# Optimization experiments

Hardware: AMD Instinct MI355X
Metric: run time of the kernel (lower is better)

## Reference

```python
import jax, jax.numpy as jnp
import numpy as np

B, L, D_MODEL, H, D_K, D_V, C = 4, 2048, 512, 8, 64, 64, 5
LN_EPS = 1e-5


def setup_inputs() -> dict:
    key = jax.random.key(0)
    ks = jax.random.split(key, 9)
    u_k = min(int(C * np.log(L)), L)  # 38
    s = 1.0 / np.sqrt(D_MODEL)
    return {
        "input_Q": jax.random.normal(ks[0], (B, L, D_MODEL), jnp.float32),
        "input_K": jax.random.normal(ks[1], (B, L, D_MODEL), jnp.float32),
        "input_V": jax.random.normal(ks[2], (B, L, D_MODEL), jnp.float32),
        "W_Q": jax.random.normal(ks[3], (D_MODEL, H * D_K), jnp.float32) * s,
        "W_K": jax.random.normal(ks[4], (D_MODEL, H * D_K), jnp.float32) * s,
        "W_V": jax.random.normal(ks[5], (D_MODEL, H * D_V), jnp.float32) * s,
        "W_fc": jax.random.normal(ks[6], (H * D_V, D_MODEL), jnp.float32) * (1.0 / np.sqrt(H * D_V)),
        "ln_gamma": jnp.ones((D_MODEL,), jnp.float32),
        "ln_beta": jnp.zeros((D_MODEL,), jnp.float32),
        "index_sample": jax.random.randint(ks[7], (L, u_k), 0, L, jnp.int32),
    }


def reference(input_Q, input_K, input_V, W_Q, W_K, W_V, W_fc, ln_gamma, ln_beta, index_sample):
    Bb, L_Q, _ = input_Q.shape
    L_K = input_K.shape[1]
    u_q = min(int(C * np.log(L_Q)), L_Q)  # n_top queries kept

    # projections -> (B, H, L, d)
    Q = (input_Q @ W_Q).reshape(Bb, L_Q, H, D_K).transpose(0, 2, 1, 3)
    K = (input_K @ W_K).reshape(Bb, L_K, H, D_K).transpose(0, 2, 1, 3)
    V = (input_V @ W_V).reshape(Bb, L_K, H, D_V).transpose(0, 2, 1, 3)

    # sampled QK scores: gather u_k random keys per query position
    K_sample = K[:, :, index_sample, :]                      # (B,H,L_Q,u_k,d_k)
    QK_sample = jnp.einsum('bhqe,bhqke->bhqk', Q, K_sample)  # (B,H,L_Q,u_k)

    # sparsity measure M = max - mean, top-u_q queries
    M = QK_sample.max(axis=-1) - QK_sample.mean(axis=-1)     # (B,H,L_Q)
    _, idx = jax.lax.top_k(M, u_q)                           # (B,H,u_q)

    # attention only for selected queries
    Q_sel = jnp.take_along_axis(Q, idx[..., None], axis=2)   # (B,H,u_q,d_k)
    scores = jnp.einsum('bhue,bhke->bhuk', Q_sel, K) / np.sqrt(D_K)
    attn = jax.nn.softmax(scores, axis=-1)
    values = jnp.einsum('bhuk,bhkd->bhud', attn, V)          # (B,H,u_q,d_v)

    # initial context = mean of V (attn_mask is None), scatter selected rows
    context = jnp.broadcast_to(V.mean(axis=2, keepdims=True), (Bb, H, L_Q, D_V))
    bb = jnp.arange(Bb)[:, None, None]
    hh = jnp.arange(H)[None, :, None]
    context = context.at[bb, hh, idx].set(values)

    context = context.transpose(0, 2, 1, 3).reshape(Bb, L_Q, H * D_V)
    out = context @ W_fc                                     # dropout p=0.0

    y = out + input_Q
    mu = y.mean(axis=-1, keepdims=True)
    var = jnp.mean(jnp.square(y - mu), axis=-1, keepdims=True)
    y = (y - mu) / jnp.sqrt(var + LN_EPS) * ln_gamma + ln_beta
    return y, idx
```

## Files before the change

kernel.cpp:

```cpp
#include <hip/hip_runtime.h>
#include <hip/hip_bf16.h>

#define NB 4
#define NL 2048
#define NH 8
#define NDM 512
#define ND 64
#define KSPLIT 4
#define QB 8

typedef __attribute__((ext_vector_type(8))) short short8b;
typedef __attribute__((ext_vector_type(4))) float f32x4;

__global__ void samp_flag_init(int* __restrict__ flag) {
  if (threadIdx.x == 0 && blockIdx.x == 0) *flag = 0;
}
__global__ void samp_probe(const int* __restrict__ sampAsInt, int* __restrict__ flag, int nwords) {
  const int g = blockIdx.x * 256 + threadIdx.x;
  if (g < nwords) {
    unsigned v = (unsigned)sampAsInt[g];
    if (v >= 2048u) atomicOr(flag, 1);
  }
}
__global__ void samp_convert(const void* __restrict__ samp, const int* __restrict__ flag,
                             int* __restrict__ sampI, int n) {
  const int g = blockIdx.x * 256 + threadIdx.x;
  if (g >= n) return;
  int v;
  if (*flag == 0) v = ((const int*)samp)[g];
  else            v = (int)(((const float*)samp)[g]);
  if (v < 0) v = 0;
  if (v > NL - 1) v = NL - 1;
  sampI[g] = v;
}

__global__ void wconv(const float* __restrict__ W, unsigned short* __restrict__ WT) {
  const int g = blockIdx.x * 256 + threadIdx.x;
  const int k = g >> 9, c = g & 511;
  __hip_bfloat16 hb = __float2bfloat16(W[(size_t)k * 512 + c]);
  WT[(size_t)c * 512 + k] = *reinterpret_cast<unsigned short*>(&hb);
}

__global__ void vmean_colmean(const float* __restrict__ inV, float* __restrict__ parts) {
  const int b = blockIdx.x, seg = blockIdx.y, t = threadIdx.x;
  const float* p = inV + ((size_t)b * NL + seg * 32) * NDM;
  float s0 = 0.f, s1 = 0.f;
  for (int r = 0; r < 32; ++r) {
    s0 += p[(size_t)r * NDM + t];
    s1 += p[(size_t)r * NDM + 256 + t];
  }
  parts[((size_t)b * 64 + seg) * NDM + t] = s0;
  parts[((size_t)b * 64 + seg) * NDM + 256 + t] = s1;
}
__global__ void vmean_gemm(const float* __restrict__ parts, const float* __restrict__ Wv,
                           float* __restrict__ Vm) {
  __shared__ float cm[512];
  const int b = blockIdx.x, t = threadIdx.x;
  float a0 = 0.f, a1 = 0.f;
  for (int g = 0; g < 64; ++g) {
    a0 += parts[((size_t)b * 64 + g) * NDM + t];
    a1 += parts[((size_t)b * 64 + g) * NDM + 256 + t];
  }
  cm[t] = a0 * (1.f / 2048.f);
  cm[t + 256] = a1 * (1.f / 2048.f);
  __syncthreads();
  const int c0 = blockIdx.y * 256 + t;
  float acc = 0.f;
  for (int k = 0; k < 512; ++k) acc += cm[k] * Wv[(size_t)k * NDM + c0];
  Vm[b * 512 + c0] = acc;
}

__global__ __launch_bounds__(256, 4) void proj3(
    const float* __restrict__ AQ, const float* __restrict__ AK,
    const float* __restrict__ wQm, const float* __restrict__ wKm,
    int gh0, float* __restrict__ Qc, float* __restrict__ Kc) {
  __shared__ float As_[32 * 132];
  __shared__ float Ws_[32 * 68];
  const int tid = threadIdx.x;
  const int bm = blockIdx.x;
  const int hl = blockIdx.y;
  const int mat = blockIdx.z;
  const int bh = gh0 + hl;
  const int b = bh >> 3, h = bh & 7;
  const float* A = (mat == 0) ? AQ : AK;
  const float* W = (mat == 0) ? wQm : wKm;
  float* D = (mat == 0) ? Qc : Kc;
  const float* Ab = A + (size_t)b * NL * NDM;
  const int colbase = h * 64;
  const int tm = tid >> 4, tn = tid & 15;
  float acc[8][4] = {};
  for (int k0 = 0; k0 < 512; k0 += 32) {
#pragma unroll
    for (int i = 0; i < 4; ++i) {
      int s = tid + i * 256;
      int r = s >> 3, c4 = (s & 7) * 4;
      float4 v = *reinterpret_cast<const float4*>(Ab + (size_t)(bm * 128 + r) * 512 + k0 + c4);
      float vv[4] = {v.x, v.y, v.z, v.w};
#pragma unroll
      for (int j = 0; j < 4; ++j) {
        int c = c4 + j;
        int rs = r ^ (((c >> 2) & 3) << 3);
        As_[c * 132 + rs] = vv[j];
      }
    }
#pragma unroll
    for (int i = 0; i < 2; ++i) {
      int s = tid + i * 256;
      int r = s >> 4, c4 = (s & 15) * 4;
      *reinterpret_cast<float4*>(&Ws_[r * 68 + c4]) =
          *reinterpret_cast<const float4*>(W + (size_t)(k0 + r) * 512 + colbase + c4);
    }
    __syncthreads();
#pragma unroll
    for (int kk = 0; kk < 32; ++kk) {
      const int sw = ((kk >> 2) & 3) << 3;
      const int mbase = (tm * 4) ^ sw;
      float4 a0 = *reinterpret_cast<const float4*>(&As_[kk * 132 + mbase]);
      float4 a1 = *reinterpret_cast<const float4*>(&As_[kk * 132 + 64 + mbase]);
      float4 w  = *reinterpret_cast<const float4*>(&Ws_[kk * 68 + tn * 4]);
      float a[8] = {a0.x, a0.y, a0.z, a0.w, a1.x, a1.y, a1.z, a1.w};
      float wv[4] = {w.x, w.y, w.z, w.w};
#pragma unroll
      for (int ii = 0; ii < 8; ++ii)
#pragma unroll
        for (int jj = 0; jj < 4; ++jj) acc[ii][jj] += a[ii] * wv[jj];
    }
    __syncthreads();
  }
#pragma unroll
  for (int ii = 0; ii < 8; ++ii) {
    int row = bm * 128 + ((ii < 4) ? (tm * 4 + ii) : (64 + tm * 4 + (ii - 4)));
    float4 v = make_float4(acc[ii][0], acc[ii][1], acc[ii][2], acc[ii][3]);
    *reinterpret_cast<float4*>(D + ((size_t)hl * NL + row) * ND + tn * 4) = v;
  }
}

__global__ __launch_bounds__(256) void projV_mfma(
    const float* __restrict__ AV, const unsigned short* __restrict__ WT,
    int gh0, float* __restrict__ Vc) {
  const int wv = threadIdx.x >> 6, l = threadIdx.x & 63;
  const int bm = blockIdx.x;
  const int hl = blockIdx.y;
  const int bh = gh0 + hl;
  const int b = bh >> 3, h = bh & 7;
  const float* Ab = AV + (size_t)b * NL * NDM;
  const int row = bm * 64 + wv * 16 + (l & 15);
  const int kg = (l >> 4) * 8;
  f32x4 acc0 = {}, acc1 = {}, acc2 = {}, acc3 = {};
  for (int k0 = 0; k0 < 512; k0 += 32) {
    const float* ap = Ab + (size_t)row * 512 + k0 + kg;
    short8b af;
#pragma unroll
    for (int j = 0; j < 8; ++j) {
      __hip_bfloat16 hb = __float2bfloat16(ap[j]);
      af[j] = *reinterpret_cast<short*>(&hb);
    }
    const unsigned short* wp = WT + (size_t)(h * 64 + (l & 15)) * 512 + k0 + kg;
    short8b b0 = *reinterpret_cast<const short8b*>(wp);
    short8b b1 = *reinterpret_cast<const short8b*>(wp + 16 * 512);
    short8b b2 = *reinterpret_cast<const short8b*>(wp + 32 * 512);
    short8b b3 = *reinterpret_cast<const short8b*>(wp + 48 * 512);
    acc0 = __builtin_amdgcn_mfma_f32_16x16x32_bf16(af, b0, acc0, 0, 0, 0);
    acc1 = __builtin_amdgcn_mfma_f32_16x16x32_bf16(af, b1, acc1, 0, 0, 0);
    acc2 = __builtin_amdgcn_mfma_f32_16x16x32_bf16(af, b2, acc2, 0, 0, 0);
    acc3 = __builtin_amdgcn_mfma_f32_16x16x32_bf16(af, b3, acc3, 0, 0, 0);
  }
  const int rbase = bm * 64 + wv * 16 + (l >> 4) * 4;
  const int col = l & 15;
#pragma unroll
  for (int j = 0; j < 4; ++j) {
    size_t o = ((size_t)hl * NL + rbase + j) * ND + col;
    Vc[o] = acc0[j];
    Vc[o + 16] = acc1[j];
    Vc[o + 32] = acc2[j];
    Vc[o + 48] = acc3[j];
  }
}

template <int UK>
__global__ __launch_bounds__(256) void sample_scores_t(
    const float* __restrict__ Q, const float* __restrict__ K,
    const int* __restrict__ sampI, float* __restrict__ M) {
  __shared__ float KsAll[4][UK * 66];
  __shared__ float QsAll[4][68];
  const int wv = threadIdx.x >> 6, l = threadIdx.x & 63;
  const int gq = blockIdx.x * 4 + wv;
  const int hl = gq >> 11;
  const int q = gq & 2047;
  float* Ks = KsAll[wv];
  float* Qs = QsAll[wv];
  const float* Kb = K + (size_t)hl * NL * ND;
  Qs[l] = Q[(size_t)gq * ND + l];
  const int base = __builtin_amdgcn_readfirstlane(q) * UK;
#pragma unroll
  for (int r = 0; r < UK; ++r) {
    int kk = sampI[base + r] & (NL - 1);
    Ks[r * 66 + l] = Kb[(size_t)kk * ND + l];
  }
  __syncthreads();
  const int myk = (l < UK) ? l : (UK - 1);
  float acc = 0.f;
#pragma unroll
  for (int j = 0; j < 32; ++j) {
    float2 kv = *reinterpret_cast<const float2*>(&Ks[myk * 66 + 2 * j]);
    float2 qv = *reinterpret_cast<const float2*>(&Qs[2 * j]);
    acc += kv.x * qv.x + kv.y * qv.y;
  }
  float mval = (l < UK) ? acc : -1e30f;
  float sval = (l < UK) ? acc : 0.f;
#pragma unroll
  for (int o = 32; o; o >>= 1) {
    mval = fmaxf(mval, __shfl_xor(mval, o, 64));
    sval += __shfl_xor(sval, o, 64);
  }
  if (l == 0) M[gq] = mval - sval * (1.f / (float)UK);
}

__global__ void sample_scores_gen(const float* __restrict__ Q, const float* __restrict__ K,
                                  const int* __restrict__ sampI, float* __restrict__ M, int uk) {
  const int wave = threadIdx.x >> 6, lane = threadIdx.x & 63;
  const int gq = blockIdx.x * 4 + wave;
  const int hl = gq >> 11;
  const int q = gq & 2047;
  const float qv = Q[(size_t)gq * ND + lane];
  const float* Kbase = K + (size_t)hl * NL * ND;
  float mx = -1e30f, sm = 0.f;
  for (int k = 0; k < uk; ++k) {
    int kidx = sampI[q * uk + k] & (NL - 1);
    float p = qv * Kbase[(size_t)kidx * ND + lane];
#pragma unroll
    for (int o = 32; o; o >>= 1) p += __shfl_xor(p, o, 64);
    mx = fmaxf(mx, p);
    sm += p;
  }
  if (lane == 0) M[gq] = mx - sm / (float)uk;
}

__global__ void topk_kernel(const float* __restrict__ M, int* __restrict__ idxo,
                            float* __restrict__ outIdx, int uq) {
  __shared__ float mv[2048];
  __shared__ float bwv[4];
  __shared__ int bwi[4];
  const int bh = blockIdx.x, t = threadIdx.x;
  for (int i = 0; i < 8; ++i) mv[t + i * 256] = M[(size_t)bh * 2048 + t + i * 256];
  __syncthreads();
  for (int it = 0; it < uq; ++it) {
    float best = -1e38f; int bidx = 1 << 30;
#pragma unroll
    for (int i = 0; i < 8; ++i) {
      int id = t + i * 256;
      float v = mv[id];
      if (v > best || (v == best && id < bidx)) { best = v; bidx = id; }
    }
#pragma unroll
    for (int o = 32; o; o >>= 1) {
      float ov = __shfl_xor(best, o, 64);
      int oi = __shfl_xor(bidx, o, 64);
      if (ov > best || (ov == best && oi < bidx)) { best = ov; bidx = oi; }
    }
    if ((t & 63) == 0) { bwv[t >> 6] = best; bwi[t >> 6] = bidx; }
    __syncthreads();
    if (t == 0) {
      float bb = bwv[0]; int bi2 = bwi[0];
#pragma unroll
      for (int w = 1; w < 4; ++w) {
        if (bwv[w] > bb || (bwv[w] == bb && bwi[w] < bi2)) { bb = bwv[w]; bi2 = bwi[w]; }
      }
      int sel = bi2 & (NL - 1);
      idxo[bh * uq + it] = sel;
      outIdx[bh * uq + it] = (float)sel;
      mv[sel] = -1e38f;
    }
    __syncthreads();
  }
}

__global__ __launch_bounds__(256) void attn_part(
    const float* __restrict__ Qw, const float* __restrict__ Kw, const float* __restrict__ Vw,
    const int* __restrict__ idxo, float* __restrict__ pacc, float* __restrict__ pml, int uq) {
  __shared__ float Qs[QB][68];
  __shared__ float Ks[64][68];
  __shared__ float Vs[64][68];
  __shared__ float sc[QB][66];
  __shared__ float accs[QB][68];
  const int hl = blockIdx.x, qg = blockIdx.y, ks = blockIdx.z;
  const int t = threadIdx.x;
#pragma unroll
  for (int i = 0; i < 2; ++i) {
    int s = t + i * 256;
    int q = s >> 6, d = s & 63;
    int u = qg * QB + q;
    float v = 0.f;
    if (u < uq) {
      int qi = idxo[hl * uq + u] & (NL - 1);
      v = Qw[((size_t)hl * NL + qi) * ND + d];
    }
    Qs[q][d] = v;
    accs[q][d] = 0.f;
  }
  float m_run = -1e30f, l_run = 0.f;
  const int q2 = t >> 5, ln = t & 31;
  __syncthreads();
  const int kbeg = ks * (NL / KSPLIT);
  for (int k0 = kbeg; k0 < kbeg + NL / KSPLIT; k0 += 64) {
#pragma unroll
    for (int i = 0; i < 4; ++i) {
      int s = t + i * 256;
      int r = s >> 4, c4 = (s & 15) * 4;
      *reinterpret_cast<float4*>(&Ks[r][c4]) =
          *reinterpret_cast<const float4*>(Kw + ((size_t)hl * NL + k0 + r) * ND + c4);
      *reinterpret_cast<float4*>(&Vs[r][c4]) =
          *reinterpret_cast<const float4*>(Vw + ((size_t)hl * NL + k0 + r) * ND + c4);
    }
    __syncthreads();
    {
      const int q = t & 7, kk = t >> 3;
      float d0 = 0.f, d1 = 0.f;
#pragma unroll
      for (int dd = 0; dd < 64; dd += 4) {
        float4 qv = *reinterpret_cast<const float4*>(&Qs[q][dd]);
        float4 ka = *reinterpret_cast<const float4*>(&Ks[kk][dd]);
        float4 kb = *reinterpret_cast<const float4*>(&Ks[kk + 32][dd]);
        d0 += qv.x * ka.x + qv.y * ka.y + qv.z * ka.z + qv.w * ka.w;
        d1 += qv.x * kb.x + qv.y * kb.y + qv.z * kb.z + qv.w * kb.w;
      }
      sc[q][kk] = d0 * 0.125f;
      sc[q][kk + 32] = d1 * 0.125f;
    }
    __syncthreads();
    {
      float s0 = sc[q2][ln], s1 = sc[q2][ln + 32];
      float tmax = fmaxf(s0, s1);
#pragma unroll
      for (int o = 16; o; o >>= 1) tmax = fmaxf(tmax, __shfl_xor(tmax, o, 64));
      float mnew = fmaxf(m_run, tmax);
      float scl = __expf(m_run - mnew);
      float p0 = __expf(s0 - mnew), p1 = __expf(s1 - mnew);
      float tsum = p0 + p1;
#pragma unroll
      for (int o = 16; o; o >>= 1) tsum += __shfl_xor(tsum, o, 64);
      l_run = l_run * scl + tsum;
      m_run = mnew;
      sc[q2][ln] = p0; sc[q2][ln + 32] = p1;
      float a0 = accs[q2][2 * ln] * scl, a1 = accs[q2][2 * ln + 1] * scl;
#pragma unroll 8
      for (int k = 0; k < 64; ++k) {
        float p = sc[q2][k];
        a0 += p * Vs[k][2 * ln];
        a1 += p * Vs[k][2 * ln + 1];
      }
      accs[q2][2 * ln] = a0; accs[q2][2 * ln + 1] = a1;
    }
    __syncthreads();
  }
  const int u = qg * QB + q2;
  if (u < uq) {
    size_t g = ((size_t)hl * uq + u) * KSPLIT + ks;
    pacc[g * ND + 2 * ln] = accs[q2][2 * ln];
    pacc[g * ND + 2 * ln + 1] = accs[q2][2 * ln + 1];
    if (ln == 0) { pml[g * 2] = m_run; pml[g * 2 + 1] = l_run; }
  }
}

__global__ void attn_merge(const float* __restrict__ pacc, const float* __restrict__ pml,
                           float* __restrict__ vals, int uq) {
  const int g = blockIdx.x;
  const int d = threadIdx.x;
  float mstar = -1e30f;
#pragma unroll
  for (int s = 0; s < KSPLIT; ++s) mstar = fmaxf(mstar, pml[((size_t)g * KSPLIT + s) * 2]);
  float num = 0.f, den = 0.f;
#pragma unroll
  for (int s = 0; s < KSPLIT; ++s) {
    float e = __expf(pml[((size_t)g * KSPLIT + s) * 2] - mstar);
    den += e * pml[((size_t)g * KSPLIT + s) * 2 + 1];
    num += e * pacc[((size_t)g * KSPLIT + s) * ND + d];
  }
  vals[(size_t)g * ND + d] = num / den;
}

__global__ void selmap_init(short* __restrict__ selmap) {
  const int g = blockIdx.x * 256 + threadIdx.x;
  selmap[g] = -1;
  selmap[g + 32768] = -1;
}
__global__ void selmap_fill(const int* __restrict__ idxo, short* __restrict__ selmap, int uq) {
  const int g = blockIdx.x * 256 + threadIdx.x;
  if (g >= NB * NH * uq) return;
  const int bh = g / uq, u = g - bh * uq;
  const int b = bh >> 3, h = bh & 7;
  const int l = idxo[g] & (NL - 1);
  selmap[((size_t)b * NL + l) * NH + h] = (short)u;
}

__global__ void base_gemm(const float* __restrict__ Vm, const float* __restrict__ Wfc,
                          float* __restrict__ base) {
  __shared__ float vm[512];
  const int b = blockIdx.x, t = threadIdx.x;
  vm[t] = Vm[b * 512 + t];
  vm[t + 256] = Vm[b * 512 + t + 256];
  __syncthreads();
  const int c0 = blockIdx.y * 256 + t;
  float acc = 0.f;
  for (int k = 0; k < 512; ++k) acc += vm[k] * Wfc[(size_t)k * 512 + c0];
  base[b * 512 + c0] = acc;
}

__global__ void corr_gemm(const float* __restrict__ vals, const float* __restrict__ Vm,
                          const float* __restrict__ Wfc, float* __restrict__ corr, int uq) {
  __shared__ float diff[64];
  const int g = blockIdx.x, t = threadIdx.x;
  const int bh = g / uq;
  const int h = bh & 7;
  if (t < 64) diff[t] = vals[(size_t)g * 64 + t] - Vm[bh * 64 + t];
  __syncthreads();
  float a0 = 0.f, a1 = 0.f;
#pragma unroll
  for (int d = 0; d < 64; ++d) {
    a0 += diff[d] * Wfc[(size_t)(h * 64 + d) * 512 + t];
    a1 += diff[d] * Wfc[(size_t)(h * 64 + d) * 512 + t + 256];
  }
  corr[(size_t)g * 512 + t] = a0;
  corr[(size_t)g * 512 + t + 256] = a1;
}

__global__ void ln_fused(const float* __restrict__ base, const float* __restrict__ resid,
                         const float* __restrict__ corr, const short* __restrict__ selmap,
                         const float* __restrict__ gamma, const float* __restrict__ beta,
                         float* __restrict__ out, int uq) {
  __shared__ float red[256];
  const int row = blockIdx.x, t = threadIdx.x;
  const int b = row >> 11;
  float y0 = base[b * 512 + t] + resid[(size_t)row * 512 + t];
  float y1 = base[b * 512 + 256 + t] + resid[(size_t)row * 512 + 256 + t];
#pragma unroll
  for (int h = 0; h < NH; ++h) {
    int s = selmap[(size_t)row * NH + h];
    if (s >= 0 && s < uq) {
      const float* cp = corr + (size_t)((b * NH + h) * uq + s) * 512;
      y0 += cp[t];
      y1 += cp[t + 256];
    }
  }
  red[t] = y0 + y1;
  __syncthreads();
  for (int s = 128; s; s >>= 1) { if (t < s) red[t] += red[t + s]; __syncthreads(); }
  const float mu = red[0] * (1.f / 512.f);
  __syncthreads();
  const float d0 = y0 - mu, d1 = y1 - mu;
  red[t] = d0 * d0 + d1 * d1;
  __syncthreads();
  for (int s = 128; s; s >>= 1) { if (t < s) red[t] += red[t + s]; __syncthreads(); }
  const float rs = rsqrtf(red[0] * (1.f / 512.f) + 1e-5f);
  __syncthreads();
  out[(size_t)row * 512 + t] = d0 * rs * gamma[t] + beta[t];
  out[(size_t)row * 512 + 256 + t] = d1 * rs * gamma[256 + t] + beta[256 + t];
}

extern "C" void kernel_launch(void* const* d_in, const int* in_sizes, int n_in,
                              void* d_out, int out_size, void* d_ws, size_t ws_size,
                              hipStream_t stream) {
  const float* inQ = (const float*)d_in[0];
  const float* inK = (const float*)d_in[1];
  const float* inV = (const float*)d_in[2];
  const float* wQ = (const float*)d_in[3];
  const float* wK = (const float*)d_in[4];
  const float* wV = (const float*)d_in[5];
  const float* wFC = (const float*)d_in[6];
  const float* gamma = (const float*)d_in[7];
  const float* beta = (const float*)d_in[8];
  const void* samp = d_in[9];

  const int nsamp = in_sizes[9];
  const int uk = nsamp / NL;
  const int uq = uk;
  const int nqg = (uq + QB - 1) / QB;

  if (out_size < NB * NL * NDM + NB * NH * uq) return;

  const size_t perH = 3 * 131072 + 2048 + (size_t)uq * KSPLIT * 64 + (size_t)uq * KSPLIT * 2;
  const size_t fixed = (size_t)32 * uq * 64 + 2048 + 2048 + (size_t)32 * uq * 512
                     + (size_t)32 * uq + 32768 + (size_t)nsamp + 131072 + 131072 + 256;
  int hcg = 0;
  for (int c = 32; c >= 1; c >>= 1) {
    if ((perH * (size_t)c + fixed + 256) * 4ull <= ws_size) { hcg = c; break; }
  }
  if (hcg == 0) return;

  float* ws = (float*)d_ws;
  float* Qc = ws;
  float* Kc = Qc + (size_t)hcg * 131072;
  float* Vc = Kc + (size_t)hcg * 131072;
  float* Mb = Vc + (size_t)hcg * 131072;
  float* pacc = Mb + (size_t)hcg * 2048;
  float* pml = pacc + (size_t)hcg * uq * KSPLIT * 64;
  float* vals = pml + (size_t)hcg * uq * KSPLIT * 2;
  float* Vm = vals + (size_t)32 * uq * 64;
  float* base = Vm + 2048;
  float* corr = base + 2048;
  int* idxo = (int*)(corr + (size_t)32 * uq * 512);
  short* selmap = (short*)(idxo + (size_t)32 * uq);
  int* sampI = (int*)(selmap + 65536);
  int* flag = sampI + nsamp;
  unsigned short* WTv = (unsigned short*)(flag + 64);
  float* vparts = (float*)(WTv + 262144);

  float* out = (float*)d_out;
  float* outIdx = out + (size_t)NB * NL * NDM;

  const int nwords = nsamp / 2;
  samp_flag_init<<<1, 64, 0, stream>>>(flag);
  samp_probe<<<(nwords + 255) / 256, 256, 0, stream>>>((const int*)samp, flag, nwords);
  samp_convert<<<(nsamp + 255) / 256, 256, 0, stream>>>(samp, flag, sampI, nsamp);
  wconv<<<1024, 256, 0, stream>>>(wV, WTv);
  vmean_colmean<<<dim3(NB, 64), 256, 0, stream>>>(inV, vparts);
  vmean_gemm<<<dim3(NB, 2), 256, 0, stream>>>(vparts, wV, Vm);

  for (int gh0 = 0; gh0 < NB * NH; gh0 += hcg) {
    proj3<<<dim3(16, hcg, 2), 256, 0, stream>>>(inQ, inK, wQ, wK, gh0, Qc, Kc);
    projV_mfma<<<dim3(32, hcg), 256, 0, stream>>>(inV, WTv, gh0, Vc);
    if (uk == 38)
      sample_scores_t<38><<<hcg * NL / 4, 256, 0, stream>>>(Qc, Kc, sampI, Mb);
    else
      sample_scores_gen<<<hcg * NL / 4, 256, 0, stream>>>(Qc, Kc, sampI, Mb, uk);
    topk_kernel<<<hcg, 256, 0, stream>>>(Mb, idxo + (size_t)gh0 * uq,
                                         outIdx + (size_t)gh0 * uq, uq);
    attn_part<<<dim3(hcg, nqg, KSPLIT), 256, 0, stream>>>(Qc, Kc, Vc,
                                                          idxo + (size_t)gh0 * uq,
                                                          pacc, pml, uq);
    attn_merge<<<hcg * uq, 64, 0, stream>>>(pacc, pml, vals + (size_t)gh0 * uq * ND, uq);
  }

  selmap_init<<<NB * NL * NH / 2 / 256, 256, 0, stream>>>(selmap);
  selmap_fill<<<(NB * NH * uq + 255) / 256, 256, 0, stream>>>(idxo, selmap, uq);
  base_gemm<<<dim3(NB, 2), 256, 0, stream>>>(Vm, wFC, base);
  corr_gemm<<<NB * NH * uq, 256, 0, stream>>>(vals, Vm, wFC, corr, uq);
  ln_fused<<<NB * NL, 256, 0, stream>>>(base, inQ, corr, selmap, gamma, beta, out, uq);
}
```

Measured before the change: 380.0 us.

## Drop sample-index conversion kernels, double attention key split, remove LDS swizzle

Removes the three preprocessing launches that checked whether index_sample was stored as int or float, clamped it and copied it. The sampling kernels now read the raw int32 input directly, masked to the valid range. Separately, KSPLIT goes from 4 to 8 to give the split-key attention more blocks, and the XOR swizzle in the proj3 shared-memory A tile is removed. Removing the swizzle may bring back LDS bank conflicts, and the larger split adds partial results for the merge kernel to combine.

```diff
diff --git a/kernel.cpp b/kernel.cpp
--- a/kernel.cpp
+++ b/kernel.cpp
@@ -6,33 +6,11 @@
 #define NH 8
 #define NDM 512
 #define ND 64
-#define KSPLIT 4
+#define KSPLIT 8
 #define QB 8
 
 typedef __attribute__((ext_vector_type(8))) short short8b;
 typedef __attribute__((ext_vector_type(4))) float f32x4;
-
-__global__ void samp_flag_init(int* __restrict__ flag) {
-  if (threadIdx.x == 0 && blockIdx.x == 0) *flag = 0;
-}
-__global__ void samp_probe(const int* __restrict__ sampAsInt, int* __restrict__ flag, int nwords) {
-  const int g = blockIdx.x * 256 + threadIdx.x;
-  if (g < nwords) {
-    unsigned v = (unsigned)sampAsInt[g];
-    if (v >= 2048u) atomicOr(flag, 1);
-  }
-}
-__global__ void samp_convert(const void* __restrict__ samp, const int* __restrict__ flag,
-                             int* __restrict__ sampI, int n) {
-  const int g = blockIdx.x * 256 + threadIdx.x;
-  if (g >= n) return;
-  int v;
-  if (*flag == 0) v = ((const int*)samp)[g];
-  else            v = (int)(((const float*)samp)[g]);
-  if (v < 0) v = 0;
-  if (v > NL - 1) v = NL - 1;
-  sampI[g] = v;
-}
 
 __global__ void wconv(const float* __restrict__ W, unsigned short* __restrict__ WT) {
   const int g = blockIdx.x * 256 + threadIdx.x;
@@ -95,13 +73,10 @@
       int s = tid + i * 256;
       int r = s >> 3, c4 = (s & 7) * 4;
       float4 v = *reinterpret_cast<const float4*>(Ab + (size_t)(bm * 128 + r) * 512 + k0 + c4);
-      float vv[4] = {v.x, v.y, v.z, v.w};
-#pragma unroll
-      for (int j = 0; j < 4; ++j) {
-        int c = c4 + j;
-        int rs = r ^ (((c >> 2) & 3) << 3);
-        As_[c * 132 + rs] = vv[j];
-      }
+      As_[(c4 + 0) * 132 + r] = v.x;
+      As_[(c4 + 1) * 132 + r] = v.y;
+      As_[(c4 + 2) * 132 + r] = v.z;
+      As_[(c4 + 3) * 132 + r] = v.w;
     }
 #pragma unroll
     for (int i = 0; i < 2; ++i) {
@@ -113,10 +88,8 @@
     __syncthreads();
 #pragma unroll
     for (int kk = 0; kk < 32; ++kk) {
-      const int sw = ((kk >> 2) & 3) << 3;
-      const int mbase = (tm * 4) ^ sw;
-      float4 a0 = *reinterpret_cast<const float4*>(&As_[kk * 132 + mbase]);
-      float4 a1 = *reinterpret_cast<const float4*>(&As_[kk * 132 + 64 + mbase]);
+      float4 a0 = *reinterpret_cast<const float4*>(&As_[kk * 132 + tm * 4]);
+      float4 a1 = *reinterpret_cast<const float4*>(&As_[kk * 132 + 64 + tm * 4]);
       float4 w  = *reinterpret_cast<const float4*>(&Ws_[kk * 68 + tn * 4]);
       float a[8] = {a0.x, a0.y, a0.z, a0.w, a1.x, a1.y, a1.z, a1.w};
       float wv[4] = {w.x, w.y, w.z, w.w};
@@ -180,7 +153,7 @@
 template <int UK>
 __global__ __launch_bounds__(256) void sample_scores_t(
     const float* __restrict__ Q, const float* __restrict__ K,
-    const int* __restrict__ sampI, float* __restrict__ M) {
+    const int* __restrict__ sampP, float* __restrict__ M) {
   __shared__ float KsAll[4][UK * 66];
   __shared__ float QsAll[4][68];
   const int wv = threadIdx.x >> 6, l = threadIdx.x & 63;
@@ -194,7 +167,7 @@
   const int base = __builtin_amdgcn_readfirstlane(q) * UK;
 #pragma unroll
   for (int r = 0; r < UK; ++r) {
-    int kk = sampI[base + r] & (NL - 1);
+    int kk = sampP[base + r] & (NL - 1);
     Ks[r * 66 + l] = Kb[(size_t)kk * ND + l];
   }
   __syncthreads();
@@ -217,7 +190,7 @@
 }
 
 __global__ void sample_scores_gen(const float* __restrict__ Q, const float* __restrict__ K,
-                                  const int* __restrict__ sampI, float* __restrict__ M, int uk) {
+                                  const int* __restrict__ sampP, float* __restrict__ M, int uk) {
   const int wave = threadIdx.x >> 6, lane = threadIdx.x & 63;
   const int gq = blockIdx.x * 4 + wave;
   const int hl = gq >> 11;
@@ -226,7 +199,7 @@
   const float* Kbase = K + (size_t)hl * NL * ND;
   float mx = -1e30f, sm = 0.f;
   for (int k = 0; k < uk; ++k) {
-    int kidx = sampI[q * uk + k] & (NL - 1);
+    int kidx = sampP[q * uk + k] & (NL - 1);
     float p = qv * Kbase[(size_t)kidx * ND + lane];
 #pragma unroll
     for (int o = 32; o; o >>= 1) p += __shfl_xor(p, o, 64);
@@ -469,7 +442,7 @@
   const float* wFC = (const float*)d_in[6];
   const float* gamma = (const float*)d_in[7];
   const float* beta = (const float*)d_in[8];
-  const void* samp = d_in[9];
+  const int* samp = (const int*)d_in[9];
 
   const int nsamp = in_sizes[9];
   const int uk = nsamp / NL;
@@ -480,7 +453,7 @@
 
   const size_t perH = 3 * 131072 + 2048 + (size_t)uq * KSPLIT * 64 + (size_t)uq * KSPLIT * 2;
   const size_t fixed = (size_t)32 * uq * 64 + 2048 + 2048 + (size_t)32 * uq * 512
-                     + (size_t)32 * uq + 32768 + (size_t)nsamp + 131072 + 131072 + 256;
+                     + (size_t)32 * uq + 32768 + 131072 + 131072 + 256;
   int hcg = 0;
   for (int c = 32; c >= 1; c >>= 1) {
     if ((perH * (size_t)c + fixed + 256) * 4ull <= ws_size) { hcg = c; break; }
@@ -500,18 +473,12 @@
   float* corr = base + 2048;
   int* idxo = (int*)(corr + (size_t)32 * uq * 512);
   short* selmap = (short*)(idxo + (size_t)32 * uq);
-  int* sampI = (int*)(selmap + 65536);
-  int* flag = sampI + nsamp;
-  unsigned short* WTv = (unsigned short*)(flag + 64);
+  unsigned short* WTv = (unsigned short*)(selmap + 65536);
   float* vparts = (float*)(WTv + 262144);
 
   float* out = (float*)d_out;
   float* outIdx = out + (size_t)NB * NL * NDM;
 
-  const int nwords = nsamp / 2;
-  samp_flag_init<<<1, 64, 0, stream>>>(flag);
-  samp_probe<<<(nwords + 255) / 256, 256, 0, stream>>>((const int*)samp, flag, nwords);
-  samp_convert<<<(nsamp + 255) / 256, 256, 0, stream>>>(samp, flag, sampI, nsamp);
   wconv<<<1024, 256, 0, stream>>>(wV, WTv);
   vmean_colmean<<<dim3(NB, 64), 256, 0, stream>>>(inV, vparts);
   vmean_gemm<<<dim3(NB, 2), 256, 0, stream>>>(vparts, wV, Vm);
@@ -520,9 +487,9 @@
     proj3<<<dim3(16, hcg, 2), 256, 0, stream>>>(inQ, inK, wQ, wK, gh0, Qc, Kc);
     projV_mfma<<<dim3(32, hcg), 256, 0, stream>>>(inV, WTv, gh0, Vc);
     if (uk == 38)
-      sample_scores_t<38><<<hcg * NL / 4, 256, 0, stream>>>(Qc, Kc, sampI, Mb);
+      sample_scores_t<38><<<hcg * NL / 4, 256, 0, stream>>>(Qc, Kc, samp, Mb);
     else
-      sample_scores_gen<<<hcg * NL / 4, 256, 0, stream>>>(Qc, Kc, sampI, Mb, uk);
+      sample_scores_gen<<<hcg * NL / 4, 256, 0, stream>>>(Qc, Kc, samp, Mb, uk);
     topk_kernel<<<hcg, 256, 0, stream>>>(Mb, idxo + (size_t)gh0 * uq,
                                          outIdx + (size_t)gh0 * uq, uq);
     attn_part<<<dim3(hcg, nqg, KSPLIT), 256, 0, stream>>>(Qc, Kc, Vc,
```

Measured after the change: 361.4 us. 1.05x faster.
